# Optimization experiments

Hardware: AMD Instinct MI355X
Metric: run time of the kernel (lower is better)

Reference implementation:

```python
import jax, jax.numpy as jnp
import numpy as np

B, S, H = 1, 4096, 3584
NQ, NKV, D = 16, 8, 256
N_REP = NQ // NKV  # GQA repeat factor = 2
WINDOW = 2048
SOFTCAP = 50.0
THETA = 10000.0
SCALE = D ** -0.5


def rotate_half(x):
    h = x.shape[-1] // 2
    return jnp.concatenate([-x[..., h:], x[..., :h]], axis=-1)


def setup_inputs() -> dict:
    key = jax.random.key(0)
    k0, k1, k2, k3, k4 = jax.random.split(key, 5)
    return {
        "hidden_states": jax.random.normal(k0, (B, S, H), jnp.float32),
        "wq": jax.random.normal(k1, (H, NQ * D), jnp.float32) / np.sqrt(H).astype(np.float32),
        "wk": jax.random.normal(k2, (H, NKV * D), jnp.float32) / np.sqrt(H).astype(np.float32),
        "wv": jax.random.normal(k3, (H, NKV * D), jnp.float32) / np.sqrt(H).astype(np.float32),
        "wo": jax.random.normal(k4, (NQ * D, H), jnp.float32) / np.sqrt(NQ * D).astype(np.float32),
        "position_ids": jnp.arange(S, dtype=jnp.int64 if jax.config.jax_enable_x64 else jnp.int32)[None, :],
    }


def reference(hidden_states, wq, wk, wv, wo, position_ids):
    b, s, h = hidden_states.shape
    # QKV projections (no bias, per attention_bias=False)
    q = (hidden_states @ wq).reshape(b, s, NQ, D).transpose(0, 2, 1, 3)   # [b, nq, s, d]
    k = (hidden_states @ wk).reshape(b, s, NKV, D).transpose(0, 2, 1, 3)  # [b, nkv, s, d]
    v = (hidden_states @ wv).reshape(b, s, NKV, D).transpose(0, 2, 1, 3)

    # Rotary embeddings (Gemma2RotaryEmbedding): freqs duplicated, rotate_half form
    pos = position_ids.astype(jnp.float32)                         # [b, s]
    inv_freq = 1.0 / (THETA ** (jnp.arange(0, D, 2, dtype=jnp.float32) / D))  # [d/2]
    freqs = pos[..., None] * inv_freq                              # [b, s, d/2]
    emb = jnp.concatenate([freqs, freqs], axis=-1)                 # [b, s, d]
    cos = jnp.cos(emb)[:, None, :, :]                              # [b, 1, s, d]
    sin = jnp.sin(emb)[:, None, :, :]
    q = q * cos + rotate_half(q) * sin
    k = k * cos + rotate_half(k) * sin

    # GQA: repeat_kv (repeat_interleave over head dim)
    k = jnp.repeat(k, N_REP, axis=1)  # [b, nq, s, d]
    v = jnp.repeat(v, N_REP, axis=1)

    # scaled scores + logit softcapping
    scores = jnp.einsum('bhqd,bhkd->bhqk', q, k) * SCALE
    scores = SOFTCAP * jnp.tanh(scores / SOFTCAP)

    # causal + sliding-window mask built from positions
    qpos = position_ids[:, None, :, None]  # [b,1,s,1]
    kpos = position_ids[:, None, None, :]  # [b,1,1,s]
    visible = (kpos <= qpos) & (kpos > qpos - WINDOW)
    scores = jnp.where(visible, scores, jnp.finfo(scores.dtype).min)

    attn = jax.nn.softmax(scores, axis=-1)
    out = jnp.einsum('bhqk,bhkd->bhqd', attn, v)      # [b, nq, s, d]
    out = out.transpose(0, 2, 1, 3).reshape(b, s, NQ * D)
    return out @ wo                                    # [b, s, h]
```

## Files before the change

kernel.cpp:

```cpp
#include <hip/hip_runtime.h>
#include <hip/hip_bf16.h>
#include <cstdint>
#include <cstddef>

#define DEVFN __device__ __forceinline__

typedef __attribute__((ext_vector_type(4))) float f32x4;
typedef __attribute__((ext_vector_type(8))) short bf16x8;
typedef __attribute__((ext_vector_type(4))) short short4v;
typedef __attribute__((ext_vector_type(8))) short short8v;

static constexpr int S = 4096;
static constexpr int H = 3584;
static constexpr int NQ = 16;
static constexpr int NKV = 8;
static constexpr int D = 256;
static constexpr int WINDOW = 2048;
static constexpr float SCALE = 0.0625f;

DEVFN unsigned short f2bf(float f) {
  union { float f; uint32_t u; } x; x.f = f;
  uint32_t u = x.u;
  u += 0x7fffu + ((u >> 16) & 1u);
  return (unsigned short)(u >> 16);
}
DEVFN float bf2f(unsigned short h) {
  union { uint32_t u; float f; } x; x.u = ((uint32_t)h) << 16;
  return x.f;
}

DEVFN void load_lds16(const void* g, void* l) {
  __builtin_amdgcn_global_load_lds((const __attribute__((address_space(1))) void*)g,
                                   (__attribute__((address_space(3))) void*)l,
                                   16, 0, 0);
}

__global__ __launch_bounds__(256) void cast_hs_kernel(const float* __restrict__ in,
                                                      unsigned short* __restrict__ out) {
  int i = (blockIdx.x * 256 + threadIdx.x) * 8;
  float4 a = *(const float4*)(in + i);
  float4 b = *(const float4*)(in + i + 4);
  short8v o;
  o[0] = (short)f2bf(a.x); o[1] = (short)f2bf(a.y);
  o[2] = (short)f2bf(a.z); o[3] = (short)f2bf(a.w);
  o[4] = (short)f2bf(b.x); o[5] = (short)f2bf(b.y);
  o[6] = (short)f2bf(b.z); o[7] = (short)f2bf(b.w);
  *(short8v*)(out + i) = o;
}

__global__ __launch_bounds__(256) void transpose_cast_kernel(const float* __restrict__ in,
                                                             unsigned short* __restrict__ out,
                                                             int rows, int cols, int out_ld) {
  __shared__ float tile[64][65];
  const int r0 = blockIdx.y * 64, c0 = blockIdx.x * 64;
  const int t = threadIdx.x;
  const int rr = t >> 4, c4 = (t & 15) * 4;
#pragma unroll
  for (int j = 0; j < 4; ++j) {
    float4 v = *(const float4*)(in + (size_t)(r0 + rr + j * 16) * cols + c0 + c4);
    tile[rr + j * 16][c4 + 0] = v.x;
    tile[rr + j * 16][c4 + 1] = v.y;
    tile[rr + j * 16][c4 + 2] = v.z;
    tile[rr + j * 16][c4 + 3] = v.w;
  }
  __syncthreads();
  const int c = t >> 2, ch = (t & 3) * 16;
  short8v o0, o1;
#pragma unroll
  for (int j = 0; j < 8; ++j) o0[j] = (short)f2bf(tile[ch + j][c]);
#pragma unroll
  for (int j = 0; j < 8; ++j) o1[j] = (short)f2bf(tile[ch + 8 + j][c]);
  unsigned short* dst = out + (size_t)(c0 + c) * out_ld + r0 + ch;
  *(short8v*)dst = o0;
  *(short8v*)(dst + 8) = o1;
}

__global__ __launch_bounds__(256) void rope_table_kernel(float* __restrict__ cs) {
  int idx = blockIdx.x * 256 + threadIdx.x;
  int s = idx >> 7, i = idx & 127;
  float inv = exp2f((float)i * -0.10381025296523007f);
  float f = (float)s * inv;
  cs[idx] = cosf(f);
  cs[(S * 128) + idx] = sinf(f);
}

__global__ __launch_bounds__(256) void rope_apply_k_kernel(unsigned short* __restrict__ k,
                                                           const float* __restrict__ cs) {
  int idx = blockIdx.x * 256 + threadIdx.x;
  int i4 = (idx & 31) * 4;
  int s = (idx >> 5) & (S - 1);
  int hh = idx >> 17;
  unsigned short* base = k + ((size_t)hh * S + s) * D;
  float4 c  = *(const float4*)(cs + (s << 7) + i4);
  float4 sn = *(const float4*)(cs + (S * 128) + (s << 7) + i4);
  short4v a = *(short4v*)(base + i4);
  short4v b = *(short4v*)(base + i4 + 128);
  short4v o1, o2;
  o1[0] = (short)f2bf(bf2f((unsigned short)a[0]) * c.x - bf2f((unsigned short)b[0]) * sn.x);
  o1[1] = (short)f2bf(bf2f((unsigned short)a[1]) * c.y - bf2f((unsigned short)b[1]) * sn.y);
  o1[2] = (short)f2bf(bf2f((unsigned short)a[2]) * c.z - bf2f((unsigned short)b[2]) * sn.z);
  o1[3] = (short)f2bf(bf2f((unsigned short)a[3]) * c.w - bf2f((unsigned short)b[3]) * sn.w);
  o2[0] = (short)f2bf(bf2f((unsigned short)b[0]) * c.x + bf2f((unsigned short)a[0]) * sn.x);
  o2[1] = (short)f2bf(bf2f((unsigned short)b[1]) * c.y + bf2f((unsigned short)a[1]) * sn.y);
  o2[2] = (short)f2bf(bf2f((unsigned short)b[2]) * c.z + bf2f((unsigned short)a[2]) * sn.z);
  o2[3] = (short)f2bf(bf2f((unsigned short)b[3]) * c.w + bf2f((unsigned short)a[3]) * sn.w);
  *(short4v*)(base + i4) = o1;
  *(short4v*)(base + i4 + 128) = o2;
}

DEVFN void gemm256_mainloop(const unsigned short* __restrict__ A,
                            const unsigned short* __restrict__ Bt,
                            int Kdim, int lda, int ldb, int row0, int col0,
                            char* lds, f32x4 acc[8][4]) {
  const int tid = threadIdx.x, lane = tid & 63;
  const int w = tid >> 6;
  const int wm = w >> 2, wn = w & 3;
  const int NT = Kdim >> 6;

  const int u = ((tid & 7) * 16) ^ (((tid >> 3) & 7) << 4);
  const int srow = (tid >> 3) + (u >> 6) * 128;
  const int sc = (u & 63) >> 1;

  const unsigned short* aSrc = A + (size_t)(row0 + srow) * lda + sc;
  const unsigned short* bSrc = Bt + (size_t)(col0 + srow) * ldb + sc;
  const size_t aj = (size_t)64 * lda, bj = (size_t)64 * ldb;

  char* const dA = lds + tid * 16;
  char* const dB = lds + 32768 + tid * 16;

  const int aoff = (lane & 15) * 128 + ((((lane >> 4) * 16) + wm * 64) ^ ((lane & 7) << 4));
  const int boff = ((wn & 1) * 64 + (lane & 15)) * 128 +
                   ((((lane >> 4) * 16) + (wn >> 1) * 64) ^ ((lane & 7) << 4));

#define STAGE_A(kt2, kh) do { \
    char* d_ = dA + (((kt2) & 1) << 16) + ((kh) << 14); \
    const unsigned short* s_ = aSrc + (kt2) * 64 + (kh) * 32; \
    load_lds16(s_, d_); load_lds16(s_ + aj, d_ + 8192); } while (0)
#define STAGE_B(kt2, kh) do { \
    char* d_ = dB + (((kt2) & 1) << 16) + ((kh) << 14); \
    const unsigned short* s_ = bSrc + (kt2) * 64 + (kh) * 32; \
    load_lds16(s_, d_); load_lds16(s_ + bj, d_ + 8192); } while (0)

  STAGE_A(0, 0); STAGE_B(0, 0); STAGE_A(0, 1); STAGE_B(0, 1);
  if (NT > 1) { STAGE_A(1, 0); STAGE_B(1, 0); }
  asm volatile("s_waitcnt vmcnt(4)" ::: "memory");
  __builtin_amdgcn_s_barrier();
  asm volatile("" ::: "memory");

  for (int kt = 0; kt < NT; ++kt) {
    const char* lA = lds + ((kt & 1) << 16) + aoff;
    const char* lB = lds + ((kt & 1) << 16) + 32768 + boff;
    bf16x8 bfr[4];
#pragma unroll
    for (int ph = 0; ph < 4; ++ph) {
      const int kh = ph >> 1;
      const int mh = ph & 1;
      bf16x8 af[4];
#pragma unroll
      for (int j = 0; j < 4; ++j)
        af[j] = *(const bf16x8*)(lA + (kh << 14) + (mh * 4 + j) * 2048);
      if (mh == 0) {
#pragma unroll
        for (int n = 0; n < 4; ++n)
          bfr[n] = *(const bf16x8*)(lB + (kh << 14) + n * 2048);
      }
      if (ph == 0)      { if (kt + 1 < NT) STAGE_A(kt + 1, 1); }
      else if (ph == 1) { if (kt + 1 < NT) STAGE_B(kt + 1, 1); }
      else if (ph == 2) { if (kt + 2 < NT) STAGE_A(kt + 2, 0); }
      else              { if (kt + 2 < NT) STAGE_B(kt + 2, 0); }

      asm volatile("" ::: "memory");
      __builtin_amdgcn_s_barrier();
      asm volatile("" ::: "memory");
      __builtin_amdgcn_s_setprio(1);
#pragma unroll
      for (int j = 0; j < 4; ++j)
#pragma unroll
        for (int n = 0; n < 4; ++n)
          acc[mh * 4 + j][n] =
              __builtin_amdgcn_mfma_f32_16x16x32_bf16(af[j], bfr[n], acc[mh * 4 + j][n], 0, 0, 0);
      __builtin_amdgcn_s_setprio(0);
      if (ph == 3) {
        if (kt < NT - 2) asm volatile("s_waitcnt vmcnt(4)" ::: "memory");
        else             asm volatile("s_waitcnt vmcnt(0)" ::: "memory");
      }
      asm volatile("" ::: "memory");
      __builtin_amdgcn_s_barrier();
      asm volatile("" ::: "memory");
    }
  }
#undef STAGE_A
#undef STAGE_B
}

__global__ __launch_bounds__(512, 2) void gemm_qkv_kernel(const unsigned short* __restrict__ A,
                                                          const unsigned short* __restrict__ Bt,
                                                          unsigned short* __restrict__ qb,
                                                          unsigned short* __restrict__ kbuf,
                                                          unsigned short* __restrict__ vtb) {
  extern __shared__ char lds[];
  int bid = blockIdx.x;
  bid = (bid & 7) * 64 + (bid >> 3);
  const int bx = bid & 15, by = bid >> 4;
  const int row0 = bx * 256, col0 = by * 256;
  f32x4 acc[8][4];
  f32x4 z = {0.f, 0.f, 0.f, 0.f};
#pragma unroll
  for (int m = 0; m < 8; ++m)
#pragma unroll
    for (int n = 0; n < 4; ++n) acc[m][n] = z;

  gemm256_mainloop(A, Bt, H, H, H, row0, col0, lds, acc);

  const int lane = threadIdx.x & 63, w = threadIdx.x >> 6;
  const int wm = w >> 2, wn = w & 3;
  const int rbase = row0 + wm * 128 + (lane >> 4) * 4;
  const int cbase = col0 + wn * 64 + (lane & 15);
  if (col0 < 4096) {
#pragma unroll
    for (int m = 0; m < 8; ++m)
#pragma unroll
      for (int n = 0; n < 4; ++n)
#pragma unroll
        for (int r = 0; r < 4; ++r) {
          int row = rbase + m * 16 + r;
          int col = cbase + n * 16;
          qb[((size_t)(col >> 8) * S + row) * D + (col & 255)] = f2bf(acc[m][n][r]);
        }
  } else if (col0 < 6144) {
#pragma unroll
    for (int m = 0; m < 8; ++m)
#pragma unroll
      for (int n = 0; n < 4; ++n)
#pragma unroll
        for (int r = 0; r < 4; ++r) {
          int row = rbase + m * 16 + r;
          int c2 = cbase + n * 16 - 4096;
          kbuf[((size_t)(c2 >> 8) * S + row) * D + (c2 & 255)] = f2bf(acc[m][n][r]);
        }
  } else {
#pragma unroll
    for (int m = 0; m < 8; ++m)
#pragma unroll
      for (int n = 0; n < 4; ++n)
#pragma unroll
        for (int r = 0; r < 4; ++r) {
          int row = rbase + m * 16 + r;
          int c3 = cbase + n * 16 - 6144;
          vtb[((size_t)(c3 >> 8) * D + (c3 & 255)) * S + row] = f2bf(acc[m][n][r]);
        }
  }
}

__global__ __launch_bounds__(512, 2) void gemm_out_kernel(const unsigned short* __restrict__ A,
                                                          const unsigned short* __restrict__ Bt,
                                                          float* __restrict__ C) {
  extern __shared__ char lds[];
  int bid = blockIdx.x;
  bid = (bid & 7) * 28 + (bid >> 3);
  const int bx = bid & 15, by = bid >> 4;
  const int row0 = bx * 256, col0 = by * 256;
  f32x4 acc[8][4];
  f32x4 z = {0.f, 0.f, 0.f, 0.f};
#pragma unroll
  for (int m = 0; m < 8; ++m)
#pragma unroll
    for (int n = 0; n < 4; ++n) acc[m][n] = z;

  gemm256_mainloop(A, Bt, NQ * D, NQ * D, NQ * D, row0, col0, lds, acc);

  const int lane = threadIdx.x & 63, w = threadIdx.x >> 6;
  const int wm = w >> 2, wn = w & 3;
  const int rbase = row0 + wm * 128 + (lane >> 4) * 4;
  const int cbase = col0 + wn * 64 + (lane & 15);
#pragma unroll
  for (int m = 0; m < 8; ++m)
#pragma unroll
    for (int n = 0; n < 4; ++n)
#pragma unroll
      for (int r = 0; r < 4; ++r)
        C[(size_t)(rbase + m * 16 + r) * H + cbase + n * 16] = acc[m][n][r];
}

__global__ __launch_bounds__(256, 2) void attn_kernel(const unsigned short* __restrict__ q,
                                                      const unsigned short* __restrict__ kk_,
                                                      const unsigned short* __restrict__ vt,
                                                      const float* __restrict__ cs,
                                                      unsigned short* __restrict__ aout) {
  __shared__ __align__(16) char kl[2][16384];
  __shared__ __align__(16) char vl[2][16384];
  __shared__ __align__(16) char pl[8192];
  const int tid = threadIdx.x, lane = tid & 63, w = tid >> 6;
  const int h = blockIdx.y, hv = h >> 1;
  const int q0 = blockIdx.x * 128;
  const int ql = lane & 15;
  const int grp = lane >> 4;
  const int qw = q0 + w * 32;

  bf16x8 qf[2][8];
#pragma unroll
  for (int qs = 0; qs < 2; ++qs) {
    const int row = qw + qs * 16 + ql;
    const unsigned short* qrow = q + ((size_t)h * S + row) * D;
#pragma unroll
    for (int t = 0; t < 8; ++t)
      qf[qs][t] = *(const bf16x8*)(qrow + t * 32 + grp * 8);
    const float* crow = cs + ((size_t)row << 7);
    const float* srow = crow + (size_t)S * 128;
#pragma unroll
    for (int t = 0; t < 4; ++t)
#pragma unroll
      for (int j = 0; j < 8; ++j) {
        const int dm = t * 32 + grp * 8 + j;
        const float c = crow[dm], s = srow[dm];
        const float lo = bf2f((unsigned short)qf[qs][t][j]);
        const float hi = bf2f((unsigned short)qf[qs][t + 4][j]);
        qf[qs][t][j]     = (short)f2bf(lo * c - hi * s);
        qf[qs][t + 4][j] = (short)f2bf(hi * c + lo * s);
      }
  }

  f32x4 oacc[2][16];
  f32x4 z = {0.f, 0.f, 0.f, 0.f};
#pragma unroll
  for (int qs = 0; qs < 2; ++qs)
#pragma unroll
    for (int i = 0; i < 16; ++i) oacc[qs][i] = z;
  float lrun[2] = {0.0f, 0.0f};

  int lo = q0 - (WINDOW - 1); if (lo < 0) lo = 0;
  const int kb0 = lo & ~31;
  const int kend = q0 + 96;

  const unsigned short* kbase = kk_ + (size_t)hv * S * D;
  const unsigned short* vbase = vt + (size_t)hv * D * S;
  int koff[4], voff[4];
#pragma unroll
  for (int j = 0; j < 4; ++j) {
    int c = w + 4 * j;
    int key = c * 2 + (lane >> 5);
    int colK = (((lane & 31) * 16) ^ ((key & 7) << 4)) >> 1;
    koff[j] = key * D + colK;
    int dd = c * 16 + (lane >> 2);
    int colV = (((lane & 3) * 16) ^ (((dd >> 1) & 3) << 4)) >> 1;
    voff[j] = dd * S + colV;
  }

  auto stage = [&](int buf, int kb) {
#pragma unroll
    for (int j = 0; j < 4; ++j) {
      int c = w + 4 * j;
      load_lds16(kbase + (size_t)kb * D + koff[j], &kl[buf][c * 1024]);
      load_lds16(vbase + kb + voff[j], &vl[buf][c * 1024]);
    }
  };

  stage(0, kb0);
  int cur = 0;
  const int psw = ((ql >> 1) & 3) << 4;
  char* pw = pl + w * 2048;
  const int ksw = (ql & 7) << 4;

  for (int kb = kb0; kb <= kend; kb += 32) {
    __syncthreads();
    if (kb + 32 <= kend) stage(cur ^ 1, kb + 32);

    f32x4 sacc[2][2];
    sacc[0][0] = z; sacc[0][1] = z; sacc[1][0] = z; sacc[1][1] = z;
#pragma unroll
    for (int t = 0; t < 8; ++t) {
      bf16x8 af[2];
#pragma unroll
      for (int ms = 0; ms < 2; ++ms)
        af[ms] = *(const bf16x8*)(kl[cur] + (ms * 16 + ql) * 512 + ((t * 64 + grp * 16) ^ ksw));
      __builtin_amdgcn_s_setprio(1);
#pragma unroll
      for (int qs = 0; qs < 2; ++qs)
#pragma unroll
        for (int ms = 0; ms < 2; ++ms)
          sacc[qs][ms] = __builtin_amdgcn_mfma_f32_16x16x32_bf16(af[ms], qf[qs][t], sacc[qs][ms], 0, 0, 0);
      __builtin_amdgcn_s_setprio(0);
    }

#pragma unroll
    for (int qs = 0; qs < 2; ++qs) {
      const int qsb = qw + qs * 16;
      const int qg = qsb + ql;
      float pv[8];
#pragma unroll
      for (int i = 0; i < 8; ++i) {
        float x = sacc[qs][i >> 2][i & 3];
        float e = __expf(x * (SCALE / 25.0f));
        float rc = __builtin_amdgcn_rcpf(e + 1.0f);
        pv[i] = __expf(rc * -100.0f);
      }
      if (kb + 31 > qsb) {
#pragma unroll
        for (int i = 0; i < 8; ++i) {
          int key = kb + (i >> 2) * 16 + grp * 4 + (i & 3);
          if (key > qg) pv[i] = 0.0f;
        }
      } else if (kb < qsb - 2032) {
#pragma unroll
        for (int i = 0; i < 8; ++i) {
          int key = kb + (i >> 2) * 16 + grp * 4 + (i & 3);
          if (key <= qg - WINDOW) pv[i] = 0.0f;
        }
      }
#pragma unroll
      for (int i = 0; i < 8; ++i) lrun[qs] += pv[i];

#pragma unroll
      for (int ms = 0; ms < 2; ++ms) {
        short4v pk;
        pk[0] = (short)f2bf(pv[ms * 4 + 0]);
        pk[1] = (short)f2bf(pv[ms * 4 + 1]);
        pk[2] = (short)f2bf(pv[ms * 4 + 2]);
        pk[3] = (short)f2bf(pv[ms * 4 + 3]);
        *(short4v*)(pw + (qs * 16 + ql) * 64 + ((ms * 32 + grp * 8) ^ psw)) = pk;
      }
    }
    asm volatile("s_waitcnt lgkmcnt(0)" ::: "memory");
    bf16x8 pb[2];
#pragma unroll
    for (int qs = 0; qs < 2; ++qs)
      pb[qs] = *(const bf16x8*)(pw + (qs * 16 + ql) * 64 + ((grp * 16) ^ psw));

#pragma unroll
    for (int nt = 0; nt < 16; ++nt) {
      int dr = nt * 16 + ql;
      bf16x8 va = *(const bf16x8*)(vl[cur] + dr * 64 + ((grp * 16) ^ (((dr >> 1) & 3) << 4)));
      __builtin_amdgcn_s_setprio(1);
      oacc[0][nt] = __builtin_amdgcn_mfma_f32_16x16x32_bf16(va, pb[0], oacc[0][nt], 0, 0, 0);
      oacc[1][nt] = __builtin_amdgcn_mfma_f32_16x16x32_bf16(va, pb[1], oacc[1][nt], 0, 0, 0);
      __builtin_amdgcn_s_setprio(0);
    }
    cur ^= 1;
  }

#pragma unroll
  for (int qs = 0; qs < 2; ++qs) {
    float l = lrun[qs];
    l += __shfl_xor(l, 16);
    l += __shfl_xor(l, 32);
    l = fmaxf(l, 1e-35f);
    float rl = 1.0f / l;
    unsigned short* orow = aout + (size_t)(qw + qs * 16 + ql) * (NQ * D) + h * D;
#pragma unroll
    for (int nt = 0; nt < 16; ++nt) {
      short4v o;
      o[0] = (short)f2bf(oacc[qs][nt][0] * rl);
      o[1] = (short)f2bf(oacc[qs][nt][1] * rl);
      o[2] = (short)f2bf(oacc[qs][nt][2] * rl);
      o[3] = (short)f2bf(oacc[qs][nt][3] * rl);
      *(short4v*)(orow + nt * 16 + grp * 4) = o;
    }
  }
}

extern "C" void kernel_launch(void* const* d_in, const int* in_sizes, int n_in,
                              void* d_out, int out_size, void* d_ws, size_t ws_size,
                              hipStream_t stream) {
  const float* hs = (const float*)d_in[0];
  const float* wq = (const float*)d_in[1];
  const float* wk = (const float*)d_in[2];
  const float* wv = (const float*)d_in[3];
  const float* wo = (const float*)d_in[4];
  float* out = (float*)d_out;

  char* ws = (char*)d_ws;
  size_t off = 0;
  auto alloc = [&](size_t bytes) {
    char* p = ws + off;
    off += (bytes + 255) & ~(size_t)255;
    return p;
  };
  unsigned short* hsb   = (unsigned short*)alloc((size_t)S * H * 2);
  unsigned short* wqkvT = (unsigned short*)alloc((size_t)8192 * H * 2);
  unsigned short* woT   = (unsigned short*)alloc((size_t)H * 4096 * 2);
  unsigned short* qb    = (unsigned short*)alloc((size_t)NQ * S * D * 2);
  unsigned short* kbuf  = (unsigned short*)alloc((size_t)NKV * S * D * 2);
  unsigned short* vtb   = (unsigned short*)alloc((size_t)NKV * D * S * 2);
  unsigned short* aob   = (unsigned short*)alloc((size_t)S * NQ * D * 2);
  float*          cs    = (float*)alloc((size_t)S * 128 * 2 * 4);
  if (off > ws_size) return;

  cast_hs_kernel<<<(S * H) / 2048, 256, 0, stream>>>(hs, hsb);
  transpose_cast_kernel<<<dim3(4096 / 64, H / 64), 256, 0, stream>>>(wq, wqkvT, H, 4096, H);
  transpose_cast_kernel<<<dim3(2048 / 64, H / 64), 256, 0, stream>>>(wk, wqkvT + (size_t)4096 * H, H, 2048, H);
  transpose_cast_kernel<<<dim3(2048 / 64, H / 64), 256, 0, stream>>>(wv, wqkvT + (size_t)6144 * H, H, 2048, H);
  transpose_cast_kernel<<<dim3(H / 64, 4096 / 64), 256, 0, stream>>>(wo, woT, 4096, H, 4096);
  rope_table_kernel<<<(S * 128) / 256, 256, 0, stream>>>(cs);
  gemm_qkv_kernel<<<512, 512, 131072, stream>>>(hsb, wqkvT, qb, kbuf, vtb);
  rope_apply_k_kernel<<<(NKV * S * 32) / 256, 256, 0, stream>>>(kbuf, cs);
  attn_kernel<<<dim3(S / 128, NQ), 256, 0, stream>>>(qb, kbuf, vtb, cs, aob);
  gemm_out_kernel<<<224, 512, 131072, stream>>>(aob, woT, out);
}
```

Before: 615.6 us.

## Split attention KV range across two blocks and combine partial outputs

Launches the attention kernel with a z-dimension of 2 so each query tile's key range is split in half and processed by two blocks. Partial unnormalized outputs and row sums go to separate buffers, and a new combine kernel adds them and normalizes. It also single-buffers V in LDS with explicit vmcnt waits and barriers, halves the P scratch, and drops setprio. The aim is more parallelism and occupancy on a grid of 512 blocks. The cost is an extra kernel, extra global traffic, and double bf16 rounding of the partial outputs.

```diff
diff --git a/kernel.cpp b/kernel.cpp
--- a/kernel.cpp
+++ b/kernel.cpp
@@ -286,17 +286,28 @@
                                                       const unsigned short* __restrict__ kk_,
                                                       const unsigned short* __restrict__ vt,
                                                       const float* __restrict__ cs,
-                                                      unsigned short* __restrict__ aout) {
+                                                      unsigned short* __restrict__ osp0,
+                                                      unsigned short* __restrict__ osp1,
+                                                      float* __restrict__ lbuf) {
   __shared__ __align__(16) char kl[2][16384];
-  __shared__ __align__(16) char vl[2][16384];
-  __shared__ __align__(16) char pl[8192];
+  __shared__ __align__(16) char vl[16384];
+  __shared__ __align__(16) char pl[4096];
   const int tid = threadIdx.x, lane = tid & 63, w = tid >> 6;
   const int h = blockIdx.y, hv = h >> 1;
+  const int sp = blockIdx.z;
   const int q0 = blockIdx.x * 128;
   const int ql = lane & 15;
   const int grp = lane >> 4;
   const int qw = q0 + w * 32;
 
+  int lo = q0 - (WINDOW - 1); if (lo < 0) lo = 0;
+  const int kb0 = lo & ~31;
+  const int kend = q0 + 96;
+  const int nt = ((kend - kb0) >> 5) + 1;
+  const int nlow = nt >> 1;
+  const int kbA = sp ? (kb0 + nlow * 32) : kb0;
+  const int kbB = sp ? kend : (kb0 + (nlow - 1) * 32);
+
   bf16x8 qf[2][8];
 #pragma unroll
   for (int qs = 0; qs < 2; ++qs) {
@@ -313,10 +324,10 @@
       for (int j = 0; j < 8; ++j) {
         const int dm = t * 32 + grp * 8 + j;
         const float c = crow[dm], s = srow[dm];
-        const float lo = bf2f((unsigned short)qf[qs][t][j]);
+        const float lo2 = bf2f((unsigned short)qf[qs][t][j]);
         const float hi = bf2f((unsigned short)qf[qs][t + 4][j]);
-        qf[qs][t][j]     = (short)f2bf(lo * c - hi * s);
-        qf[qs][t + 4][j] = (short)f2bf(hi * c + lo * s);
+        qf[qs][t][j]     = (short)f2bf(lo2 * c - hi * s);
+        qf[qs][t + 4][j] = (short)f2bf(hi * c + lo2 * s);
       }
   }
 
@@ -327,10 +338,6 @@
 #pragma unroll
     for (int i = 0; i < 16; ++i) oacc[qs][i] = z;
   float lrun[2] = {0.0f, 0.0f};
-
-  int lo = q0 - (WINDOW - 1); if (lo < 0) lo = 0;
-  const int kb0 = lo & ~31;
-  const int kend = q0 + 96;
 
   const unsigned short* kbase = kk_ + (size_t)hv * S * D;
   const unsigned short* vbase = vt + (size_t)hv * D * S;
@@ -346,24 +353,30 @@
     voff[j] = dd * S + colV;
   }
 
-  auto stage = [&](int buf, int kb) {
-#pragma unroll
-    for (int j = 0; j < 4; ++j) {
-      int c = w + 4 * j;
-      load_lds16(kbase + (size_t)kb * D + koff[j], &kl[buf][c * 1024]);
-      load_lds16(vbase + kb + voff[j], &vl[buf][c * 1024]);
-    }
+  auto stageK = [&](int buf, int kb) {
+#pragma unroll
+    for (int j = 0; j < 4; ++j)
+      load_lds16(kbase + (size_t)kb * D + koff[j], &kl[buf][(w + 4 * j) * 1024]);
   };
-
-  stage(0, kb0);
+  auto stageV = [&](int kb) {
+#pragma unroll
+    for (int j = 0; j < 4; ++j)
+      load_lds16(vbase + kb + voff[j], &vl[(w + 4 * j) * 1024]);
+  };
+
+  stageK(0, kbA);
+  stageV(kbA);
   int cur = 0;
   const int psw = ((ql >> 1) & 3) << 4;
-  char* pw = pl + w * 2048;
+  char* pw = pl + w * 1024;
   const int ksw = (ql & 7) << 4;
 
-  for (int kb = kb0; kb <= kend; kb += 32) {
-    __syncthreads();
-    if (kb + 32 <= kend) stage(cur ^ 1, kb + 32);
+  for (int kb = kbA; kb <= kbB; kb += 32) {
+    const bool more = (kb + 32 <= kbB);
+    asm volatile("s_waitcnt vmcnt(4)" ::: "memory");
+    __builtin_amdgcn_s_barrier();
+    asm volatile("" ::: "memory");
+    if (more) stageK(cur ^ 1, kb + 32);
 
     f32x4 sacc[2][2];
     sacc[0][0] = z; sacc[0][1] = z; sacc[1][0] = z; sacc[1][1] = z;
@@ -373,15 +386,14 @@
 #pragma unroll
       for (int ms = 0; ms < 2; ++ms)
         af[ms] = *(const bf16x8*)(kl[cur] + (ms * 16 + ql) * 512 + ((t * 64 + grp * 16) ^ ksw));
-      __builtin_amdgcn_s_setprio(1);
 #pragma unroll
       for (int qs = 0; qs < 2; ++qs)
 #pragma unroll
         for (int ms = 0; ms < 2; ++ms)
           sacc[qs][ms] = __builtin_amdgcn_mfma_f32_16x16x32_bf16(af[ms], qf[qs][t], sacc[qs][ms], 0, 0, 0);
-      __builtin_amdgcn_s_setprio(0);
     }
 
+    bf16x8 pb[2];
 #pragma unroll
     for (int qs = 0; qs < 2; ++qs) {
       const int qsb = qw + qs * 16;
@@ -417,45 +429,69 @@
         pk[1] = (short)f2bf(pv[ms * 4 + 1]);
         pk[2] = (short)f2bf(pv[ms * 4 + 2]);
         pk[3] = (short)f2bf(pv[ms * 4 + 3]);
-        *(short4v*)(pw + (qs * 16 + ql) * 64 + ((ms * 32 + grp * 8) ^ psw)) = pk;
+        *(short4v*)(pw + ql * 64 + ((ms * 32 + grp * 8) ^ psw)) = pk;
       }
+      asm volatile("s_waitcnt lgkmcnt(0)" ::: "memory");
+      pb[qs] = *(const bf16x8*)(pw + ql * 64 + ((grp * 16) ^ psw));
+      asm volatile("s_waitcnt lgkmcnt(0)" ::: "memory");
     }
-    asm volatile("s_waitcnt lgkmcnt(0)" ::: "memory");
-    bf16x8 pb[2];
-#pragma unroll
-    for (int qs = 0; qs < 2; ++qs)
-      pb[qs] = *(const bf16x8*)(pw + (qs * 16 + ql) * 64 + ((grp * 16) ^ psw));
-
-#pragma unroll
-    for (int nt = 0; nt < 16; ++nt) {
-      int dr = nt * 16 + ql;
-      bf16x8 va = *(const bf16x8*)(vl[cur] + dr * 64 + ((grp * 16) ^ (((dr >> 1) & 3) << 4)));
-      __builtin_amdgcn_s_setprio(1);
-      oacc[0][nt] = __builtin_amdgcn_mfma_f32_16x16x32_bf16(va, pb[0], oacc[0][nt], 0, 0, 0);
-      oacc[1][nt] = __builtin_amdgcn_mfma_f32_16x16x32_bf16(va, pb[1], oacc[1][nt], 0, 0, 0);
-      __builtin_amdgcn_s_setprio(0);
+
+    if (more) asm volatile("s_waitcnt vmcnt(4)" ::: "memory");
+    else      asm volatile("s_waitcnt vmcnt(0)" ::: "memory");
+    __builtin_amdgcn_s_barrier();
+    asm volatile("" ::: "memory");
+
+#pragma unroll
+    for (int nt2 = 0; nt2 < 16; ++nt2) {
+      int dr = nt2 * 16 + ql;
+      bf16x8 va = *(const bf16x8*)(vl + dr * 64 + ((grp * 16) ^ (((dr >> 1) & 3) << 4)));
+      oacc[0][nt2] = __builtin_amdgcn_mfma_f32_16x16x32_bf16(va, pb[0], oacc[0][nt2], 0, 0, 0);
+      oacc[1][nt2] = __builtin_amdgcn_mfma_f32_16x16x32_bf16(va, pb[1], oacc[1][nt2], 0, 0, 0);
     }
+
+    asm volatile("" ::: "memory");
+    __builtin_amdgcn_s_barrier();
+    asm volatile("" ::: "memory");
+    if (more) stageV(kb + 32);
     cur ^= 1;
   }
 
+  unsigned short* osp = sp ? osp1 : osp0;
 #pragma unroll
   for (int qs = 0; qs < 2; ++qs) {
     float l = lrun[qs];
     l += __shfl_xor(l, 16);
     l += __shfl_xor(l, 32);
-    l = fmaxf(l, 1e-35f);
-    float rl = 1.0f / l;
-    unsigned short* orow = aout + (size_t)(qw + qs * 16 + ql) * (NQ * D) + h * D;
-#pragma unroll
-    for (int nt = 0; nt < 16; ++nt) {
+    const int row = qw + qs * 16 + ql;
+    if (grp == 0) lbuf[((size_t)sp * NQ + h) * S + row] = l;
+    unsigned short* orow = osp + (size_t)row * (NQ * D) + h * D;
+#pragma unroll
+    for (int nt2 = 0; nt2 < 16; ++nt2) {
       short4v o;
-      o[0] = (short)f2bf(oacc[qs][nt][0] * rl);
-      o[1] = (short)f2bf(oacc[qs][nt][1] * rl);
-      o[2] = (short)f2bf(oacc[qs][nt][2] * rl);
-      o[3] = (short)f2bf(oacc[qs][nt][3] * rl);
-      *(short4v*)(orow + nt * 16 + grp * 4) = o;
+      o[0] = (short)f2bf(oacc[qs][nt2][0]);
+      o[1] = (short)f2bf(oacc[qs][nt2][1]);
+      o[2] = (short)f2bf(oacc[qs][nt2][2]);
+      o[3] = (short)f2bf(oacc[qs][nt2][3]);
+      *(short4v*)(orow + nt2 * 16 + grp * 4) = o;
     }
   }
+}
+
+__global__ __launch_bounds__(256) void attn_combine_kernel(unsigned short* __restrict__ o0,
+                                                           const unsigned short* __restrict__ o1,
+                                                           const float* __restrict__ lbuf) {
+  size_t base = ((size_t)blockIdx.x * 256 + threadIdx.x) * 8;
+  const int row = (int)(base >> 12);
+  const int h = (int)((base >> 8) & 15);
+  float l = lbuf[(size_t)h * S + row] + lbuf[(size_t)(NQ + h) * S + row];
+  float rl = 1.0f / fmaxf(l, 1e-35f);
+  short8v a = *(const short8v*)(o0 + base);
+  short8v b = *(const short8v*)(o1 + base);
+  short8v o;
+#pragma unroll
+  for (int j = 0; j < 8; ++j)
+    o[j] = (short)f2bf((bf2f((unsigned short)a[j]) + bf2f((unsigned short)b[j])) * rl);
+  *(short8v*)(o0 + base) = o;
 }
 
 extern "C" void kernel_launch(void* const* d_in, const int* in_sizes, int n_in,
@@ -482,6 +518,8 @@
   unsigned short* kbuf  = (unsigned short*)alloc((size_t)NKV * S * D * 2);
   unsigned short* vtb   = (unsigned short*)alloc((size_t)NKV * D * S * 2);
   unsigned short* aob   = (unsigned short*)alloc((size_t)S * NQ * D * 2);
+  unsigned short* aob1  = (unsigned short*)alloc((size_t)S * NQ * D * 2);
+  float*          lbuf  = (float*)alloc((size_t)2 * NQ * S * 4);
   float*          cs    = (float*)alloc((size_t)S * 128 * 2 * 4);
   if (off > ws_size) return;
 
@@ -493,6 +531,7 @@
   rope_table_kernel<<<(S * 128) / 256, 256, 0, stream>>>(cs);
   gemm_qkv_kernel<<<512, 512, 131072, stream>>>(hsb, wqkvT, qb, kbuf, vtb);
   rope_apply_k_kernel<<<(NKV * S * 32) / 256, 256, 0, stream>>>(kbuf, cs);
-  attn_kernel<<<dim3(S / 128, NQ), 256, 0, stream>>>(qb, kbuf, vtb, cs, aob);
+  attn_kernel<<<dim3(S / 128, NQ, 2), 256, 0, stream>>>(qb, kbuf, vtb, cs, aob, aob1, lbuf);
+  attn_combine_kernel<<<(S * NQ * D) / 2048, 256, 0, stream>>>(aob, aob1, lbuf);
   gemm_out_kernel<<<224, 512, 131072, stream>>>(aob, woT, out);
 }
```

After: 695.9 us. +13.0%, slower.
